# Kernel tuning notes

Hardware: AMD Instinct MI355X
Metric: run time of the kernel (lower is better)

## Reference

```python
import jax, jax.numpy as jnp
import numpy as np

A, B = 1024, 1024
NODE_DIM, EDGE_DIM = 32, 16
EDGE_IN = 2 * NODE_DIM + 2 * EDGE_DIM  # 96
NODE_IN = NODE_DIM + EDGE_DIM          # 48


def setup_inputs() -> dict:
    key = jax.random.key(0)
    ks = jax.random.split(key, 11)
    s = lambda *sh: 1.0 / np.sqrt(sh[0])
    return {
        "edge_embeds": jax.random.normal(ks[0], (A, B, 2 * EDGE_DIM), dtype=jnp.float32),
        "nodes_a_embeds": jax.random.normal(ks[1], (A, NODE_DIM), dtype=jnp.float32),
        "nodes_b_embeds": jax.random.normal(ks[2], (B, NODE_DIM), dtype=jnp.float32),
        # edge_mlp params
        "W1e": jax.random.uniform(ks[3], (EDGE_IN, EDGE_DIM), jnp.float32, -s(EDGE_IN), s(EDGE_IN)),
        "b1e": jax.random.uniform(ks[4], (EDGE_DIM,), jnp.float32, -s(EDGE_IN), s(EDGE_IN)),
        "W2e": jax.random.uniform(ks[5], (EDGE_DIM, EDGE_DIM), jnp.float32, -s(EDGE_DIM), s(EDGE_DIM)),
        "b2e": jax.random.uniform(ks[6], (EDGE_DIM,), jnp.float32, -s(EDGE_DIM), s(EDGE_DIM)),
        # node_mlp params
        "W1n": jax.random.uniform(ks[7], (NODE_IN, NODE_DIM), jnp.float32, -s(NODE_IN), s(NODE_IN)),
        "b1n": jax.random.uniform(ks[8], (NODE_DIM,), jnp.float32, -s(NODE_IN), s(NODE_IN)),
        "W2n": jax.random.uniform(ks[9], (NODE_DIM, NODE_DIM), jnp.float32, -s(NODE_DIM), s(NODE_DIM)),
        "b2n": jax.random.uniform(ks[10], (NODE_DIM,), jnp.float32, -s(NODE_DIM), s(NODE_DIM)),
    }


def reference(edge_embeds, nodes_a_embeds, nodes_b_embeds,
              W1e, b1e, W2e, b2e, W1n, b1n, W2n, b2n):
    ed = 2 * EDGE_DIM
    # Edge update. concat(edge, na_bcast, nb_bcast) @ W1e decomposed into three
    # matmuls added via broadcasting (same math, no repeat/concat materialized).
    We, Wa, Wb = W1e[:ed], W1e[ed:ed + NODE_DIM], W1e[ed + NODE_DIM:]
    h = (jnp.einsum('abe,ed->abd', edge_embeds, We)
         + (nodes_a_embeds @ Wa)[:, None, :]
         + (nodes_b_embeds @ Wb)[None, :, :]
         + b1e)                                  # (A, B, edge_dim)
    h = jax.nn.relu(h)
    edge_latent = jax.nn.relu(h @ W2e + b2e)     # (A, B, edge_dim)

    # Node update: sum-reduce edges, concat with node embeds, shared MLP.
    a_in = jnp.concatenate([nodes_a_embeds, edge_latent.sum(axis=1)], axis=1)
    b_in = jnp.concatenate([nodes_b_embeds, edge_latent.sum(axis=0)], axis=1)
    node_mlp = lambda x: jax.nn.relu(jax.nn.relu(x @ W1n + b1n) @ W2n + b2n)
    return edge_latent, node_mlp(a_in), node_mlp(b_in)
```

## Files before the change

kernel.cpp:

```cpp
#include <hip/hip_runtime.h>

#define A_DIM 1024
#define B_DIM 1024

typedef __attribute__((ext_vector_type(8))) short bfrag8;
typedef __attribute__((ext_vector_type(4))) float facc4;

__device__ __forceinline__ unsigned short f2bf(float f) {
    unsigned u = __float_as_uint(f);
    u = (u + 0x7FFFu + ((u >> 16) & 1u)) >> 16;
    return (unsigned short)u;
}
__device__ __forceinline__ unsigned cvtpk(float lo, float hi) {
    unsigned r;
    asm("v_cvt_pk_bf16_f32 %0, %1, %2" : "=v"(r) : "v"(lo), "v"(hi));
    return r;
}

__global__ __launch_bounds__(256) void prep_kernel(
    const float* __restrict__ na, const float* __restrict__ nb,
    const float* __restrict__ W1e, const float* __restrict__ b1e,
    float* __restrict__ ha, float* __restrict__ hb)
{
    int idx = blockIdx.x * 256 + threadIdx.x;
    int half = idx >> 14;
    int r = (idx >> 4) & 1023;
    int d = idx & 15;
    const float* x = (half ? nb : na) + r * 32;
    const float* W = W1e + (half ? 64 * 16 : 32 * 16) + d;
    float acc = half ? 0.f : b1e[d];
    #pragma unroll
    for (int k = 0; k < 32; ++k) acc += x[k] * W[k * 16];
    (half ? hb : ha)[r * 16 + d] = acc;
}

__global__ __launch_bounds__(512, 4) void edge_kernel(
    const float* __restrict__ E, const float* __restrict__ W1e,
    const float* __restrict__ W2e, const float* __restrict__ b2e,
    const float* __restrict__ ha, const float* __restrict__ hb,
    float* __restrict__ el_out, float* __restrict__ suma_p,
    float* __restrict__ sumb_p)
{
    __shared__ __align__(16) float smem[8704];
    const int tid  = threadIdx.x;
    const int lane = tid & 63;
    const int w    = tid >> 6;
    const int n    = lane & 15;
    const int g    = lane >> 4;
    const int bg   = blockIdx.x;
    const int at   = blockIdx.y;
    const int bbase = bg * 64;
    const int abase = at * 32;

    smem[8192 + tid] = ha[abase * 16 + tid];
    __syncthreads();

    bfrag8 w1f, w2f;
    #pragma unroll
    for (int t = 0; t < 8; ++t) {
        w1f[t] = (short)f2bf(W1e[(g * 8 + t) * 16 + n]);
        w2f[t] = (g < 2) ? (short)f2bf(W2e[(g * 8 + t) * 16 + n]) : (short)0;
    }
    facc4 hbF[4];
    #pragma unroll
    for (int mt = 0; mt < 4; ++mt)
        hbF[mt] = *(const facc4*)&hb[(bbase + mt * 16 + n) * 16 + g * 4];
    facc4 b2f = *(const facc4*)&b2e[g * 4];

    facc4 sumbA[4];
    #pragma unroll
    for (int mt = 0; mt < 4; ++mt) sumbA[mt] = facc4{0.f, 0.f, 0.f, 0.f};

    char* sbase = (char*)smem + w * 4096;
    const int q3 = lane >> 3, jj = lane & 7;
    char* wptr = sbase + q3 * 64 + ((((jj >> 1) ^ (q3 >> 1)) & 3) << 4) + ((jj & 1) << 3);
    const char* rptr = sbase + n * 64 + ((g ^ ((n >> 1) & 3)) << 4);

    float4 gbuf[8];
    {
        const float4* p = (const float4*)(E + ((size_t)(abase + w * 4) * B_DIM + bbase) * 32);
        #pragma unroll
        for (int t = 0; t < 8; ++t) gbuf[t] = p[t * 64 + lane];
    }

    #pragma unroll
    for (int i = 0; i < 4; ++i) {
        const int a = abase + w * 4 + i;

        #pragma unroll
        for (int t = 0; t < 8; ++t) {
            unsigned lo = cvtpk(gbuf[t].x, gbuf[t].y);
            unsigned hi = cvtpk(gbuf[t].z, gbuf[t].w);
            *(uint2*)(wptr + t * 512) = make_uint2(lo, hi);
        }
        if (i < 3) {
            const float4* p = (const float4*)(E + ((size_t)(a + 1) * B_DIM + bbase) * 32);
            #pragma unroll
            for (int t = 0; t < 8; ++t) gbuf[t] = p[t * 64 + lane];
        }

        facc4 haf = *(const facc4*)&smem[8192 + (w * 4 + i) * 16 + g * 4];

        facc4 acc[4];
        #pragma unroll
        for (int mt = 0; mt < 4; ++mt) {
            bfrag8 ef = *(const bfrag8*)(rptr + mt * 1024);
            acc[mt] = __builtin_amdgcn_mfma_f32_16x16x32_bf16(
                w1f, ef, haf + hbF[mt], 0, 0, 0);
        }

        facc4 ssum = facc4{0.f, 0.f, 0.f, 0.f};
        #pragma unroll
        for (int mt = 0; mt < 4; ++mt) {
            facc4 h = acc[mt];
            h.x = fmaxf(h.x, 0.f); h.y = fmaxf(h.y, 0.f);
            h.z = fmaxf(h.z, 0.f); h.w = fmaxf(h.w, 0.f);
            const int sl = (n + g * 32) & 63;
            const int sh = (n + g * 32 + 16) & 63;
            float v0 = __shfl(h.x, sl), v1 = __shfl(h.y, sl);
            float v2 = __shfl(h.z, sl), v3 = __shfl(h.w, sl);
            float u0 = __shfl(h.x, sh), u1 = __shfl(h.y, sh);
            float u2 = __shfl(h.z, sh), u3 = __shfl(h.w, sh);
            union { unsigned u[4]; bfrag8 s; } bb;
            bb.u[0] = cvtpk(v0, v1); bb.u[1] = cvtpk(v2, v3);
            bb.u[2] = cvtpk(u0, u1); bb.u[3] = cvtpk(u2, u3);
            facc4 e = __builtin_amdgcn_mfma_f32_16x16x32_bf16(w2f, bb.s, b2f, 0, 0, 0);
            e.x = fmaxf(e.x, 0.f); e.y = fmaxf(e.y, 0.f);
            e.z = fmaxf(e.z, 0.f); e.w = fmaxf(e.w, 0.f);
            *(facc4*)&el_out[((size_t)a * B_DIM + bbase + mt * 16 + n) * 16 + g * 4] = e;
            sumbA[mt] += e;
            ssum += e;
        }
        #pragma unroll
        for (int m = 1; m <= 8; m <<= 1) {
            ssum.x += __shfl_xor(ssum.x, m);
            ssum.y += __shfl_xor(ssum.y, m);
            ssum.z += __shfl_xor(ssum.z, m);
            ssum.w += __shfl_xor(ssum.w, m);
        }
        if (n == 0)
            *(facc4*)&suma_p[((size_t)bg * A_DIM + a) * 16 + g * 4] = ssum;
    }

    __syncthreads();
    #pragma unroll
    for (int mt = 0; mt < 4; ++mt)
        ((facc4*)smem)[(w * 64 + mt * 16 + n) * 4 + g] = sumbA[mt];
    __syncthreads();
    if (tid < 256) {
        const int bl = tid >> 2, q = tid & 3;
        facc4 s = facc4{0.f, 0.f, 0.f, 0.f};
        #pragma unroll
        for (int ww = 0; ww < 8; ++ww) s += ((facc4*)smem)[(ww * 64 + bl) * 4 + q];
        *(facc4*)&sumb_p[((size_t)at * B_DIM + bbase + bl) * 16 + q * 4] = s;
    }
}

__global__ __launch_bounds__(256) void reduce_kernel(
    const float* __restrict__ suma_p, const float* __restrict__ sumb_p,
    float* __restrict__ suma, float* __restrict__ sumb)
{
    int idx = blockIdx.x * 256 + threadIdx.x;
    if (idx < 16384) {
        float acc = 0.f;
        #pragma unroll
        for (int t = 0; t < 16; ++t) acc += suma_p[t * 16384 + idx];
        suma[idx] = acc;
    } else {
        int j = idx - 16384;
        float acc = 0.f;
        #pragma unroll
        for (int t = 0; t < 32; ++t) acc += sumb_p[t * 16384 + j];
        sumb[j] = acc;
    }
}

__global__ __launch_bounds__(256) void node_kernel(
    const float* __restrict__ na, const float* __restrict__ nb,
    const float* __restrict__ suma, const float* __restrict__ sumb,
    const float* __restrict__ W1n, const float* __restrict__ b1n,
    const float* __restrict__ W2n, const float* __restrict__ b2n,
    float* __restrict__ out_a, float* __restrict__ out_b)
{
    __shared__ float W1_s[48 * 32];
    __shared__ float W2_s[32 * 32];
    __shared__ float hid_s[8][32];
    int tid = threadIdx.x;
    for (int i = tid; i < 1536; i += 256) W1_s[i] = W1n[i];
    for (int i = tid; i < 1024; i += 256) W2_s[i] = W2n[i];
    __syncthreads();
    int rlocal = tid >> 5;
    int r = blockIdx.x * 8 + rlocal;
    int j = tid & 31;
    int isb = (r >= 1024);
    int rr = isb ? r - 1024 : r;
    const float* nx = (isb ? nb : na) + rr * 32;
    const float* sx = (isb ? sumb : suma) + rr * 16;
    float acc = b1n[j];
    #pragma unroll
    for (int k = 0; k < 32; ++k) acc += nx[k] * W1_s[k * 32 + j];
    #pragma unroll
    for (int k = 0; k < 16; ++k) acc += sx[k] * W1_s[(32 + k) * 32 + j];
    hid_s[rlocal][j] = fmaxf(acc, 0.f);
    __syncthreads();
    float acc2 = b2n[j];
    #pragma unroll
    for (int k = 0; k < 32; ++k) acc2 += hid_s[rlocal][k] * W2_s[k * 32 + j];
    (isb ? out_b : out_a)[rr * 32 + j] = fmaxf(acc2, 0.f);
}

extern "C" void kernel_launch(void* const* d_in, const int* in_sizes, int n_in,
                              void* d_out, int out_size, void* d_ws, size_t ws_size,
                              hipStream_t stream)
{
    const float* E   = (const float*)d_in[0];
    const float* na  = (const float*)d_in[1];
    const float* nb  = (const float*)d_in[2];
    const float* W1e = (const float*)d_in[3];
    const float* b1e = (const float*)d_in[4];
    const float* W2e = (const float*)d_in[5];
    const float* b2e = (const float*)d_in[6];
    const float* W1n = (const float*)d_in[7];
    const float* b1n = (const float*)d_in[8];
    const float* W2n = (const float*)d_in[9];
    const float* b2n = (const float*)d_in[10];

    float* out    = (float*)d_out;
    float* el_out = out;
    float* out_a  = out + (size_t)A_DIM * B_DIM * 16;
    float* out_b  = out_a + A_DIM * 32;

    float* ws     = (float*)d_ws;
    float* ha     = ws;
    float* hb     = ws + 16384;
    float* suma_p = ws + 32768;
    float* sumb_p = suma_p + 16 * 16384;
    float* suma   = sumb_p + 32 * 16384;
    float* sumb   = suma + 16384;

    hipLaunchKernelGGL(prep_kernel, dim3(128), dim3(256), 0, stream,
                       na, nb, W1e, b1e, ha, hb);
    hipLaunchKernelGGL(edge_kernel, dim3(16, 32), dim3(512), 0, stream,
                       E, W1e, W2e, b2e, ha, hb, el_out, suma_p, sumb_p);
    hipLaunchKernelGGL(reduce_kernel, dim3(128), dim3(256), 0, stream,
                       suma_p, sumb_p, suma, sumb);
    hipLaunchKernelGGL(node_kernel, dim3(256), dim3(256), 0, stream,
                       na, nb, suma, sumb, W1n, b1n, W2n, b2n, out_a, out_b);
}
```

Before: 58.71 us.

## Load edges directly into MFMA fragments, double block size, fold reduce into node kernel

The edge kernel no longer stages edge embeddings through LDS with a software prefetch. Each lane loads its bf16 B-fragment straight from global memory, and the block grows to 1024 threads, with each wave handling 2 rows instead of 4. The B-side partial sums are now reduced in LDS across 16 waves in two stages. The separate reduce kernel is removed and its partial-sum reduction moves into node_kernel, saving one launch. The trade-off is uncoalesced 32-byte-per-lane global loads with no explicit prefetch, and a serial partial-sum loop inside the node kernel.

After: 71.36 us. 1.22x slower.

```diff
diff --git a/kernel.cpp b/kernel.cpp
--- a/kernel.cpp
+++ b/kernel.cpp
@@ -34,14 +34,14 @@
     (half ? hb : ha)[r * 16 + d] = acc;
 }
 
-__global__ __launch_bounds__(512, 4) void edge_kernel(
+__global__ __launch_bounds__(1024, 8) void edge_kernel(
     const float* __restrict__ E, const float* __restrict__ W1e,
     const float* __restrict__ W2e, const float* __restrict__ b2e,
     const float* __restrict__ ha, const float* __restrict__ hb,
     float* __restrict__ el_out, float* __restrict__ suma_p,
     float* __restrict__ sumb_p)
 {
-    __shared__ __align__(16) float smem[8704];
+    __shared__ __align__(16) float sb[8 * 64 * 16];
     const int tid  = threadIdx.x;
     const int lane = tid & 63;
     const int w    = tid >> 6;
@@ -52,69 +52,39 @@
     const int bbase = bg * 64;
     const int abase = at * 32;
 
-    smem[8192 + tid] = ha[abase * 16 + tid];
-    __syncthreads();
-
     bfrag8 w1f, w2f;
     #pragma unroll
     for (int t = 0; t < 8; ++t) {
         w1f[t] = (short)f2bf(W1e[(g * 8 + t) * 16 + n]);
         w2f[t] = (g < 2) ? (short)f2bf(W2e[(g * 8 + t) * 16 + n]) : (short)0;
     }
-    facc4 hbF[4];
-    #pragma unroll
-    for (int mt = 0; mt < 4; ++mt)
-        hbF[mt] = *(const facc4*)&hb[(bbase + mt * 16 + n) * 16 + g * 4];
     facc4 b2f = *(const facc4*)&b2e[g * 4];
 
     facc4 sumbA[4];
     #pragma unroll
     for (int mt = 0; mt < 4; ++mt) sumbA[mt] = facc4{0.f, 0.f, 0.f, 0.f};
 
-    char* sbase = (char*)smem + w * 4096;
-    const int q3 = lane >> 3, jj = lane & 7;
-    char* wptr = sbase + q3 * 64 + ((((jj >> 1) ^ (q3 >> 1)) & 3) << 4) + ((jj & 1) << 3);
-    const char* rptr = sbase + n * 64 + ((g ^ ((n >> 1) & 3)) << 4);
-
-    float4 gbuf[8];
-    {
-        const float4* p = (const float4*)(E + ((size_t)(abase + w * 4) * B_DIM + bbase) * 32);
-        #pragma unroll
-        for (int t = 0; t < 8; ++t) gbuf[t] = p[t * 64 + lane];
-    }
-
-    #pragma unroll
-    for (int i = 0; i < 4; ++i) {
-        const int a = abase + w * 4 + i;
-
-        #pragma unroll
-        for (int t = 0; t < 8; ++t) {
-            unsigned lo = cvtpk(gbuf[t].x, gbuf[t].y);
-            unsigned hi = cvtpk(gbuf[t].z, gbuf[t].w);
-            *(uint2*)(wptr + t * 512) = make_uint2(lo, hi);
-        }
-        if (i < 3) {
-            const float4* p = (const float4*)(E + ((size_t)(a + 1) * B_DIM + bbase) * 32);
-            #pragma unroll
-            for (int t = 0; t < 8; ++t) gbuf[t] = p[t * 64 + lane];
-        }
-
-        facc4 haf = *(const facc4*)&smem[8192 + (w * 4 + i) * 16 + g * 4];
-
-        facc4 acc[4];
+    #pragma unroll
+    for (int i = 0; i < 2; ++i) {
+        const int a = abase + w * 2 + i;
+        facc4 haf = *(const facc4*)&ha[a * 16 + g * 4];
+        facc4 ssum = facc4{0.f, 0.f, 0.f, 0.f};
+
         #pragma unroll
         for (int mt = 0; mt < 4; ++mt) {
-            bfrag8 ef = *(const bfrag8*)(rptr + mt * 1024);
-            acc[mt] = __builtin_amdgcn_mfma_f32_16x16x32_bf16(
-                w1f, ef, haf + hbF[mt], 0, 0, 0);
-        }
-
-        facc4 ssum = facc4{0.f, 0.f, 0.f, 0.f};
-        #pragma unroll
-        for (int mt = 0; mt < 4; ++mt) {
-            facc4 h = acc[mt];
+            const float* ep = E + ((size_t)a * B_DIM + bbase + mt * 16 + n) * 32 + g * 8;
+            float4 lo = *(const float4*)ep;
+            float4 hi = *(const float4*)(ep + 4);
+            union { unsigned u[4]; bfrag8 s; } ef;
+            ef.u[0] = cvtpk(lo.x, lo.y); ef.u[1] = cvtpk(lo.z, lo.w);
+            ef.u[2] = cvtpk(hi.x, hi.y); ef.u[3] = cvtpk(hi.z, hi.w);
+
+            facc4 hbf = *(const facc4*)&hb[(bbase + mt * 16 + n) * 16 + g * 4];
+            facc4 h = __builtin_amdgcn_mfma_f32_16x16x32_bf16(
+                w1f, ef.s, haf + hbf, 0, 0, 0);
             h.x = fmaxf(h.x, 0.f); h.y = fmaxf(h.y, 0.f);
             h.z = fmaxf(h.z, 0.f); h.w = fmaxf(h.w, 0.f);
+
             const int sl = (n + g * 32) & 63;
             const int sh = (n + g * 32 + 16) & 63;
             float v0 = __shfl(h.x, sl), v1 = __shfl(h.y, sl);
@@ -124,9 +94,11 @@
             union { unsigned u[4]; bfrag8 s; } bb;
             bb.u[0] = cvtpk(v0, v1); bb.u[1] = cvtpk(v2, v3);
             bb.u[2] = cvtpk(u0, u1); bb.u[3] = cvtpk(u2, u3);
+
             facc4 e = __builtin_amdgcn_mfma_f32_16x16x32_bf16(w2f, bb.s, b2f, 0, 0, 0);
             e.x = fmaxf(e.x, 0.f); e.y = fmaxf(e.y, 0.f);
             e.z = fmaxf(e.z, 0.f); e.w = fmaxf(e.w, 0.f);
+
             *(facc4*)&el_out[((size_t)a * B_DIM + bbase + mt * 16 + n) * 16 + g * 4] = e;
             sumbA[mt] += e;
             ssum += e;
@@ -143,41 +115,32 @@
     }
 
     __syncthreads();
-    #pragma unroll
-    for (int mt = 0; mt < 4; ++mt)
-        ((facc4*)smem)[(w * 64 + mt * 16 + n) * 4 + g] = sumbA[mt];
+    if (w >= 8) {
+        #pragma unroll
+        for (int mt = 0; mt < 4; ++mt)
+            ((facc4*)sb)[((w - 8) * 64 + mt * 16 + n) * 4 + g] = sumbA[mt];
+    }
+    __syncthreads();
+    if (w < 8) {
+        #pragma unroll
+        for (int mt = 0; mt < 4; ++mt) {
+            sumbA[mt] += ((facc4*)sb)[(w * 64 + mt * 16 + n) * 4 + g];
+            ((facc4*)sb)[(w * 64 + mt * 16 + n) * 4 + g] = sumbA[mt];
+        }
+    }
     __syncthreads();
     if (tid < 256) {
         const int bl = tid >> 2, q = tid & 3;
         facc4 s = facc4{0.f, 0.f, 0.f, 0.f};
         #pragma unroll
-        for (int ww = 0; ww < 8; ++ww) s += ((facc4*)smem)[(ww * 64 + bl) * 4 + q];
+        for (int ww = 0; ww < 8; ++ww) s += ((facc4*)sb)[(ww * 64 + bl) * 4 + q];
         *(facc4*)&sumb_p[((size_t)at * B_DIM + bbase + bl) * 16 + q * 4] = s;
-    }
-}
-
-__global__ __launch_bounds__(256) void reduce_kernel(
-    const float* __restrict__ suma_p, const float* __restrict__ sumb_p,
-    float* __restrict__ suma, float* __restrict__ sumb)
-{
-    int idx = blockIdx.x * 256 + threadIdx.x;
-    if (idx < 16384) {
-        float acc = 0.f;
-        #pragma unroll
-        for (int t = 0; t < 16; ++t) acc += suma_p[t * 16384 + idx];
-        suma[idx] = acc;
-    } else {
-        int j = idx - 16384;
-        float acc = 0.f;
-        #pragma unroll
-        for (int t = 0; t < 32; ++t) acc += sumb_p[t * 16384 + j];
-        sumb[j] = acc;
     }
 }
 
 __global__ __launch_bounds__(256) void node_kernel(
     const float* __restrict__ na, const float* __restrict__ nb,
-    const float* __restrict__ suma, const float* __restrict__ sumb,
+    const float* __restrict__ suma_p, const float* __restrict__ sumb_p,
     const float* __restrict__ W1n, const float* __restrict__ b1n,
     const float* __restrict__ W2n, const float* __restrict__ b2n,
     float* __restrict__ out_a, float* __restrict__ out_b)
@@ -185,22 +148,29 @@
     __shared__ float W1_s[48 * 32];
     __shared__ float W2_s[32 * 32];
     __shared__ float hid_s[8][32];
+    __shared__ float sx_s[8][16];
     int tid = threadIdx.x;
     for (int i = tid; i < 1536; i += 256) W1_s[i] = W1n[i];
     for (int i = tid; i < 1024; i += 256) W2_s[i] = W2n[i];
-    __syncthreads();
     int rlocal = tid >> 5;
     int r = blockIdx.x * 8 + rlocal;
     int j = tid & 31;
     int isb = (r >= 1024);
     int rr = isb ? r - 1024 : r;
+    if (j < 16) {
+        const float* P = isb ? sumb_p : suma_p;
+        int np = isb ? 32 : 16;
+        float acc = 0.f;
+        for (int t = 0; t < np; ++t) acc += P[(size_t)t * 16384 + rr * 16 + j];
+        sx_s[rlocal][j] = acc;
+    }
+    __syncthreads();
     const float* nx = (isb ? nb : na) + rr * 32;
-    const float* sx = (isb ? sumb : suma) + rr * 16;
     float acc = b1n[j];
     #pragma unroll
     for (int k = 0; k < 32; ++k) acc += nx[k] * W1_s[k * 32 + j];
     #pragma unroll
-    for (int k = 0; k < 16; ++k) acc += sx[k] * W1_s[(32 + k) * 32 + j];
+    for (int k = 0; k < 16; ++k) acc += sx_s[rlocal][k] * W1_s[(32 + k) * 32 + j];
     hid_s[rlocal][j] = fmaxf(acc, 0.f);
     __syncthreads();
     float acc2 = b2n[j];
@@ -235,15 +205,11 @@
     float* hb     = ws + 16384;
     float* suma_p = ws + 32768;
     float* sumb_p = suma_p + 16 * 16384;
-    float* suma   = sumb_p + 32 * 16384;
-    float* sumb   = suma + 16384;
 
     hipLaunchKernelGGL(prep_kernel, dim3(128), dim3(256), 0, stream,
                        na, nb, W1e, b1e, ha, hb);
-    hipLaunchKernelGGL(edge_kernel, dim3(16, 32), dim3(512), 0, stream,
+    hipLaunchKernelGGL(edge_kernel, dim3(16, 32), dim3(1024), 0, stream,
                        E, W1e, W2e, b2e, ha, hb, el_out, suma_p, sumb_p);
-    hipLaunchKernelGGL(reduce_kernel, dim3(128), dim3(256), 0, stream,
-                       suma_p, sumb_p, suma, sumb);
     hipLaunchKernelGGL(node_kernel, dim3(256), dim3(256), 0, stream,
-                       na, nb, suma, sumb, W1n, b1n, W2n, b2n, out_a, out_b);
-}
+                       na, nb, suma_p, sumb_p, W1n, b1n, W2n, b2n, out_a, out_b);
+}
```
